# Optimization experiments

Hardware: AMD Instinct MI355X
Metric: run time of the kernel (lower is better)

Reference implementation:

```python
import jax, jax.numpy as jnp
import numpy as np
from jax import lax

K, INC, OUC = 6, 64, 32
H, W = 512, 512
WIN = 128  # min(128, min(H,W)) for training path
ITERATION = 2  # torch uses random.randint(1,3); fixed for determinism


def setup_inputs() -> dict:
    key = jax.random.key(0)
    ks = jax.random.split(key, 12)
    s = 0.05
    return {
        "x": jax.random.uniform(ks[0], (K, 3, H, W), jnp.float32),
        "pred_list": jax.random.uniform(ks[1], (K, 3, H, W), jnp.float32),
        "feat_list": jax.random.normal(ks[2], (K, INC, H, W), jnp.float32) * 0.1,
        "split_w": jax.random.normal(ks[3], (3 * OUC, INC, 3, 3), jnp.float32) * s,
        "split_b": jax.random.normal(ks[4], (3 * OUC,), jnp.float32) * s,
        "merge1_w": jax.random.normal(ks[5], (INC, 3 * OUC + 3, 3, 3), jnp.float32) * s,
        "merge1_b": jax.random.normal(ks[6], (INC,), jnp.float32) * s,
        "merge2_w": jax.random.normal(ks[7], (INC, INC, 3, 3), jnp.float32) * s,
        "merge2_b": jax.random.normal(ks[8], (INC,), jnp.float32) * s,
        "head_w": jax.random.normal(ks[9], (3, INC, 3, 3), jnp.float32) * s,
        "head_b": jax.random.normal(ks[10], (3,), jnp.float32) * s,
    }


def _conv(x, w, b, groups=1):
    y = lax.conv_general_dilated(
        x, w, (1, 1), ((1, 1), (1, 1)),
        dimension_numbers=("NCHW", "OIHW", "NCHW"), feature_group_count=groups)
    return y + b[None, :, None, None]


def _get_box(pred_list):
    # B_cat = mean of bg channel, T_cat = sum of fg channel; distance map [H,W]
    B_cat = pred_list[:, 2].mean(axis=0)
    T_cat = pred_list[:, 0].sum(axis=0)
    distance = jnp.abs(1.0 - T_cat - B_cat)
    # nearest-neighbor downsample by 0.1: out[i,j] = in[10*i, 10*j]
    hs, ws = H // 10, W // 10
    ds = distance[::10, ::10][:hs, :ws]
    # NMS keep[0] (training path uses boxes[0:1]) == global argmax of score
    idx = jnp.argmax(ds.reshape(-1))
    cx = (idx % ws) * 10
    cy = (idx // ws) * 10
    half = WIN // 2
    x1, y1 = cx - half, cy - half
    x2, y2 = cx + half, cy + half
    ox = (-jnp.minimum(x1, 0) + jnp.minimum(W - x1, 0)
          - jnp.minimum(x2, 0) + jnp.minimum(W - x2, 0))
    oy = (-jnp.minimum(y1, 0) + jnp.minimum(H - y1, 0)
          - jnp.minimum(y2, 0) + jnp.minimum(H - y2, 0))
    return (y1 + oy).astype(jnp.int32), (x1 + ox).astype(jnp.int32)


def reference(x, pred_list, feat_list, split_w, split_b,
              merge1_w, merge1_b, merge2_w, merge2_b, head_w, head_b):
    c = INC
    y1, x1 = _get_box(pred_list)  # box fixed across iterations (computed once)
    x_patch = lax.dynamic_slice(x, (0, 0, y1, x1), (K, 3, WIN, WIN))
    feat_patch = lax.dynamic_slice(feat_list, (0, 0, y1, x1), (K, INC, WIN, WIN))
    feat_tiled = jnp.tile(feat_patch, (1, 3, 1, 1))
    denom = max(K - 1, 1)

    pl = pred_list
    for _ in range(ITERATION):
        pred_patch = lax.dynamic_slice(pl, (0, 0, y1, x1), (K, 3, WIN, WIN))
        # cat([p0.repeat(c), p1.repeat(c), p2.repeat(c)]) == repeat each channel c times
        attention = jnp.repeat(pred_patch, c, axis=1)
        fs = _conv(feat_tiled * attention, split_w, split_b, groups=3)
        f0, f1, f2 = fs[:, :OUC], fs[:, OUC:2 * OUC], fs[:, 2 * OUC:]
        feat_t = f1.sum(0, keepdims=True) / denom - f0.sum(0, keepdims=True) + 2.0 * f0
        feat_r = f0.sum(0, keepdims=True) - f0 + f1
        feat_b = jnp.broadcast_to(f2.mean(0, keepdims=True), f2.shape)
        fcat = jnp.concatenate([feat_t, feat_r, feat_b, x_patch], axis=1)
        h1 = jax.nn.leaky_relu(_conv(fcat, merge1_w, merge1_b), 0.2)
        fm = _conv(h1, merge2_w, merge2_b)
        pr = _conv(fm, head_w, head_b)
        inner = (jnp.tanh(pr[:, :, 10:WIN - 10, 10:WIN - 10]) + 1.0) / 2.0
        pl = lax.dynamic_update_slice(pl, inner, (0, 0, y1 + 10, x1 + 10))
    return pl
```

## Files before the change

### kernel.cpp

```cpp
#include <hip/hip_runtime.h>
#include <math.h>

typedef __attribute__((ext_vector_type(8))) short short8_t;
typedef __attribute__((ext_vector_type(4))) float f32x4;

#define Hh 512
#define Ww 512
#define IMG (Hh * Ww)
#define WINP 128
#define PP (WINP * WINP)
#define QS 325

__device__ __forceinline__ unsigned short f2bf(float f) {
    unsigned int u = __builtin_bit_cast(unsigned int, f);
    u += 0x7fffu + ((u >> 16) & 1u);
    return (unsigned short)(u >> 16);
}
__device__ __forceinline__ float bf2f(unsigned short h) {
    unsigned int u = ((unsigned int)h) << 16;
    return __builtin_bit_cast(float, u);
}

__global__ void prologue_kernel(const float* __restrict__ pred, int* __restrict__ box,
                                const float* __restrict__ sw, const float* __restrict__ m1w,
                                const float* __restrict__ m2w, const float* __restrict__ hw,
                                unsigned short* __restrict__ WF,
                                const float4* __restrict__ csrc, float4* __restrict__ cdst)
{
    int b = blockIdx.x;
    int tid = threadIdx.x;
    if (b < 684) {
        int idx = b * 256 + tid;
        int j = idx & 7;
        int lane = (idx >> 3) & 63;
        int frag = idx >> 9;
        int n16 = lane & 15;
        int ko = (lane >> 4) * 8 + j;
        float v = 0.f;
        if (frag < 108) {
            int g = frag / 36; int r = frag % 36; int kc = r / 18; r %= 18; int tap = r / 2; int nf = r & 1;
            int oc = g * 32 + nf * 16 + n16; int ic = kc * 32 + ko;
            v = sw[(oc * 64 + ic) * 9 + tap];
        } else if (frag < 252) {
            int r = frag - 108; int half = r / 72; r %= 72; int kc = r / 18; r %= 18; int tap = r / 2; int nf = r & 1;
            int oc = half * 32 + nf * 16 + n16; int ic = kc * 32 + ko;
            if (ic < 99) v = m1w[(oc * 99 + ic) * 9 + tap];
        } else if (frag < 324) {
            int r = frag - 252; int half = r / 36; r %= 36; int kc = r / 18; r %= 18; int tap = r / 2; int nf = r & 1;
            int oc = half * 32 + nf * 16 + n16; int ic = kc * 32 + ko;
            v = m2w[(oc * 64 + ic) * 9 + tap];
        } else {
            int r = frag - 324; int kc = r / 9; int tap = r % 9;
            int ic = kc * 32 + ko;
            if (n16 < 3) v = hw[(n16 * 64 + ic) * 9 + tap];
        }
        WF[idx] = f2bf(v);
        return;
    }
    if (b < 5292) {
        int i = (b - 684) * 256 + tid;
        cdst[i] = csrc[i];
        return;
    }
    float best = -1.0f; int bidx = 0x7fffffff;
    for (int cand = tid; cand < 51 * 51; cand += 256) {
        int i = cand / 51, jj = cand % 51;
        int y = i * 10, x = jj * 10;
        float T = 0.f, Bv = 0.f;
#pragma unroll
        for (int k = 0; k < 6; ++k) {
            T  += pred[((k * 3 + 0) * Hh + y) * Ww + x];
            Bv += pred[((k * 3 + 2) * Hh + y) * Ww + x];
        }
        float d = fabsf(1.0f - T - Bv / 6.0f);
        if (d > best || (d == best && cand < bidx)) { best = d; bidx = cand; }
    }
    __shared__ float sv[256];
    __shared__ int   si[256];
    sv[tid] = best; si[tid] = bidx;
    __syncthreads();
    for (int s = 128; s > 0; s >>= 1) {
        if (tid < s) {
            if (sv[tid + s] > sv[tid] || (sv[tid + s] == sv[tid] && si[tid + s] < si[tid])) {
                sv[tid] = sv[tid + s]; si[tid] = si[tid + s];
            }
        }
        __syncthreads();
    }
    if (tid == 0) {
        int idx = si[0];
        int cy = (idx / 51) * 10, cx = (idx % 51) * 10;
        int yy = cy - 64; yy = yy < 0 ? 0 : (yy > Hh - WINP ? Hh - WINP : yy);
        int xx = cx - 64; xx = xx < 0 ? 0 : (xx > Ww - WINP ? Ww - WINP : xx);
        box[0] = yy; box[1] = xx;
    }
}

__global__ void prep_featcl(const float* __restrict__ feat, const int* __restrict__ box,
                            unsigned short* __restrict__ featcl)
{
    int row = blockIdx.x;
    int k = blockIdx.y;
    int t = threadIdx.x;
    int y1 = box[0], x1 = box[1];
    __shared__ unsigned short s[128 * 64];
    for (int i = 0; i < 32; ++i) {
        int idx = t + i * 256;
        int ic = idx >> 7, c = idx & 127;
        s[c * 64 + ic] = f2bf(feat[((size_t)(k * 64 + ic) * Hh + y1 + row) * Ww + x1 + c]);
    }
    __syncthreads();
    if (t < 128) {
        unsigned short* dst = &featcl[((size_t)k * 16384 + row * 128 + t) * 64];
        for (int i = 0; i < 8; ++i)
            *(short8_t*)&dst[i * 8] = *(short8_t*)&s[t * 64 + i * 8];
    }
}


__global__ __launch_bounds__(256) void split_mfma(
    const unsigned short* __restrict__ featcl, const float* __restrict__ pl,
    const unsigned short* __restrict__ WF, const float* __restrict__ sb,
    const int* __restrict__ box, unsigned short* __restrict__ fscl)
{
    const int tid = threadIdx.x;
    const int l = tid & 63, w = tid >> 6;
    const int T = blockIdx.x;
    const int k = blockIdx.y / 3, g = blockIdx.y % 3;
    const int ty0 = (T >> 3) * 16, tx0 = (T & 7) * 16;
    const int y1 = box[0], x1 = box[1];
    const int nf = w & 1;
    const int rbase = (w >> 1) * 8;

    __shared__ __align__(16) unsigned short s_a[4 * QS * 8];
    __shared__ __align__(16) unsigned short s_b[9216];

    f32x4 acc[8];
#pragma unroll
    for (int mf = 0; mf < 8; ++mf) acc[mf] = (f32x4){0.f, 0.f, 0.f, 0.f};

    const float* plg = pl + (size_t)(k * 3 + g) * IMG + (size_t)y1 * Ww + x1;
    const unsigned short* fck = featcl + (size_t)k * 16384 * 64;

    for (int kc = 0; kc < 2; ++kc) {
        __syncthreads();
#pragma unroll
        for (int i = 0; i < 6; ++i) {
            int s = tid + i * 256;
            if (s < 1296) {
                int pxs = s >> 2, q = s & 3;
                int r = pxs / 18, c = pxs - r * 18;
                int py = ty0 - 1 + r, px = tx0 - 1 + c;
                short8_t o;
                if (py >= 0 && py < WINP && px >= 0 && px < WINP) {
                    float pv = plg[py * Ww + px];
                    short8_t f = *(const short8_t*)&fck[(size_t)(py * WINP + px) * 64 + kc * 32 + q * 8];
#pragma unroll
                    for (int e = 0; e < 8; ++e) o[e] = (short)f2bf(bf2f((unsigned short)f[e]) * pv);
                } else {
#pragma unroll
                    for (int e = 0; e < 8; ++e) o[e] = 0;
                }
                *(short8_t*)&s_a[(q * QS + pxs) * 8] = o;
            }
        }
        {
            const unsigned short* src = WF + (size_t)((g * 2 + kc) * 18) * 512;
#pragma unroll
            for (int i = 0; i < 5; ++i) {
                int cch = tid + i * 256;
                if (cch < 1152)
                    *(short8_t*)&s_b[cch * 8] = *(const short8_t*)&src[cch * 8];
            }
        }
        __syncthreads();
        short8_t breg[9];
#pragma unroll
        for (int tap = 0; tap < 9; ++tap)
            breg[tap] = *(const short8_t*)&s_b[((tap * 2 + nf) * 64 + l) * 8];
#pragma unroll
        for (int r = 0; r < 10; ++r) {
            short8_t av[3];
#pragma unroll
            for (int dx = 0; dx < 3; ++dx)
                av[dx] = *(const short8_t*)&s_a[((l >> 4) * QS + (rbase + r) * 18 + (l & 15) + dx) * 8];
#pragma unroll
            for (int dy = 0; dy < 3; ++dy) {
                const int mf = r - dy;
                if (mf >= 0 && mf < 8) {
#pragma unroll
                    for (int dx = 0; dx < 3; ++dx)
                        acc[mf] = __builtin_amdgcn_mfma_f32_16x16x32_bf16(av[dx], breg[dy * 3 + dx], acc[mf], 0, 0, 0);
                }
            }
        }
    }
    __syncthreads();
    unsigned short* s_t = s_a;
    {
        float bias = sb[g * 32 + nf * 16 + (l & 15)];
        int slot = nf * 2 + ((l & 15) >> 3);
#pragma unroll
        for (int mf = 0; mf < 8; ++mf) {
            int row = rbase + mf;
#pragma unroll
            for (int r = 0; r < 4; ++r) {
                int col = (l >> 4) * 4 + r;
                s_t[(slot * 256 + row * 16 + col) * 8 + (l & 7)] = f2bf(acc[mf][r] + bias);
            }
        }
    }
    __syncthreads();
    {
        int row = tid >> 4, col = tid & 15;
        size_t gpx = (size_t)(ty0 + row) * WINP + tx0 + col;
        unsigned short* dst = fscl + ((size_t)k * 16384 + gpx) * 96 + g * 32;
#pragma unroll
        for (int i = 0; i < 4; ++i)
            *(short8_t*)&dst[i * 8] = *(short8_t*)&s_t[(i * 256 + tid) * 8];
    }
}

__global__ void reduce_kernel(const unsigned short* __restrict__ fscl, float* __restrict__ Scl)
{
    int tg = blockIdx.x * 256 + threadIdx.x;
    int px = tg >> 2, q = tg & 3;
    float s0[8], s1[8], s2[8];
#pragma unroll
    for (int e = 0; e < 8; ++e) { s0[e] = 0.f; s1[e] = 0.f; s2[e] = 0.f; }
#pragma unroll
    for (int k = 0; k < 6; ++k) {
        const unsigned short* p = &fscl[((size_t)k * 16384 + px) * 96 + q * 8];
        short8_t a0 = *(const short8_t*)&p[0];
        short8_t a1 = *(const short8_t*)&p[32];
        short8_t a2 = *(const short8_t*)&p[64];
#pragma unroll
        for (int e = 0; e < 8; ++e) {
            s0[e] += bf2f((unsigned short)a0[e]);
            s1[e] += bf2f((unsigned short)a1[e]);
            s2[e] += bf2f((unsigned short)a2[e]);
        }
    }
    float* d = &Scl[(size_t)px * 96 + q * 8];
#pragma unroll
    for (int e = 0; e < 8; ++e) {
        d[e]      = s1[e] * 0.2f - s0[e];
        d[32 + e] = s0[e];
        d[64 + e] = s2[e] * (1.f / 6.f);
    }
}

__global__ __launch_bounds__(256) void merge1_mfma(
    const unsigned short* __restrict__ fscl, const float* __restrict__ Scl,
    const float* __restrict__ x, const unsigned short* __restrict__ WF,
    const float* __restrict__ m1b, const int* __restrict__ box,
    unsigned short* __restrict__ h1cl)
{
    const int tid = threadIdx.x;
    const int l = tid & 63, w = tid >> 6;
    const int T = blockIdx.x;
    const int k = blockIdx.y >> 1, half = blockIdx.y & 1;
    const int ty0 = (T >> 3) * 16, tx0 = (T & 7) * 16;
    const int y1 = box[0], x1 = box[1];
    const int nf = w & 1;
    const int rbase = (w >> 1) * 8;

    __shared__ __align__(16) unsigned short s_a[4 * QS * 8];
    __shared__ __align__(16) unsigned short s_b[9216];

    f32x4 acc[8];
#pragma unroll
    for (int mf = 0; mf < 8; ++mf) acc[mf] = (f32x4){0.f, 0.f, 0.f, 0.f};

    for (int kc = 0; kc < 4; ++kc) {
        __syncthreads();
#pragma unroll
        for (int i = 0; i < 6; ++i) {
            int s = tid + i * 256;
            if (s < 1296) {
                int pxs = s >> 2, q = s & 3;
                int r = pxs / 18, c = pxs - r * 18;
                int py = ty0 - 1 + r, px = tx0 - 1 + c;
                short8_t o;
#pragma unroll
                for (int e = 0; e < 8; ++e) o[e] = 0;
                if (py >= 0 && py < WINP && px >= 0 && px < WINP) {
                    size_t gpx = (size_t)py * WINP + px;
                    if (kc == 0) {
                        short8_t f0 = *(const short8_t*)&fscl[((size_t)k * 16384 + gpx) * 96 + q * 8];
                        const float* S = &Scl[gpx * 96 + q * 8];
#pragma unroll
                        for (int e = 0; e < 8; ++e)
                            o[e] = (short)f2bf(S[e] + 2.f * bf2f((unsigned short)f0[e]));
                    } else if (kc == 1) {
                        const unsigned short* fp = &fscl[((size_t)k * 16384 + gpx) * 96];
                        short8_t f0 = *(const short8_t*)&fp[q * 8];
                        short8_t f1 = *(const short8_t*)&fp[32 + q * 8];
                        const float* S = &Scl[gpx * 96 + 32 + q * 8];
#pragma unroll
                        for (int e = 0; e < 8; ++e)
                            o[e] = (short)f2bf(S[e] - bf2f((unsigned short)f0[e]) + bf2f((unsigned short)f1[e]));
                    } else if (kc == 2) {
                        const float* S = &Scl[gpx * 96 + 64 + q * 8];
#pragma unroll
                        for (int e = 0; e < 8; ++e) o[e] = (short)f2bf(S[e]);
                    } else {
                        if (q == 0) {
#pragma unroll
                            for (int ch = 0; ch < 3; ++ch)
                                o[ch] = (short)f2bf(x[(size_t)(k * 3 + ch) * IMG + (size_t)(y1 + py) * Ww + x1 + px]);
                        }
                    }
                }
                *(short8_t*)&s_a[(q * QS + pxs) * 8] = o;
            }
        }
        {
            const unsigned short* src = WF + (size_t)(108 + (half * 4 + kc) * 18) * 512;
#pragma unroll
            for (int i = 0; i < 5; ++i) {
                int cch = tid + i * 256;
                if (cch < 1152)
                    *(short8_t*)&s_b[cch * 8] = *(const short8_t*)&src[cch * 8];
            }
        }
        __syncthreads();
        short8_t breg[9];
#pragma unroll
        for (int tap = 0; tap < 9; ++tap)
            breg[tap] = *(const short8_t*)&s_b[((tap * 2 + nf) * 64 + l) * 8];
#pragma unroll
        for (int r = 0; r < 10; ++r) {
            short8_t av[3];
#pragma unroll
            for (int dx = 0; dx < 3; ++dx)
                av[dx] = *(const short8_t*)&s_a[((l >> 4) * QS + (rbase + r) * 18 + (l & 15) + dx) * 8];
#pragma unroll
            for (int dy = 0; dy < 3; ++dy) {
                const int mf = r - dy;
                if (mf >= 0 && mf < 8) {
#pragma unroll
                    for (int dx = 0; dx < 3; ++dx)
                        acc[mf] = __builtin_amdgcn_mfma_f32_16x16x32_bf16(av[dx], breg[dy * 3 + dx], acc[mf], 0, 0, 0);
                }
            }
        }
    }
    __syncthreads();
    unsigned short* s_t = s_a;
    {
        float bias = m1b[half * 32 + nf * 16 + (l & 15)];
        int slot = nf * 2 + ((l & 15) >> 3);
#pragma unroll
        for (int mf = 0; mf < 8; ++mf) {
            int row = rbase + mf;
#pragma unroll
            for (int r = 0; r < 4; ++r) {
                int col = (l >> 4) * 4 + r;
                float v = acc[mf][r] + bias;
                v = v >= 0.f ? v : 0.2f * v;
                s_t[(slot * 256 + row * 16 + col) * 8 + (l & 7)] = f2bf(v);
            }
        }
    }
    __syncthreads();
    {
        int row = tid >> 4, col = tid & 15;
        size_t gpx = (size_t)(ty0 + row) * WINP + tx0 + col;
        unsigned short* dst = h1cl + ((size_t)k * 16384 + gpx) * 64 + half * 32;
#pragma unroll
        for (int i = 0; i < 4; ++i)
            *(short8_t*)&dst[i * 8] = *(short8_t*)&s_t[(i * 256 + tid) * 8];
    }
}

__global__ __launch_bounds__(256) void merge2_mfma(
    const unsigned short* __restrict__ h1cl, const unsigned short* __restrict__ WF,
    const float* __restrict__ m2b, unsigned short* __restrict__ h2cl)
{
    const int tid = threadIdx.x;
    const int l = tid & 63, w = tid >> 6;
    const int T = blockIdx.x;
    const int k = blockIdx.y >> 1, half = blockIdx.y & 1;
    const int ty0 = (T >> 3) * 16, tx0 = (T & 7) * 16;
    const int nf = w & 1;
    const int rbase = (w >> 1) * 8;

    __shared__ __align__(16) unsigned short s_a[4 * QS * 8];
    __shared__ __align__(16) unsigned short s_b[9216];

    f32x4 acc[8];
#pragma unroll
    for (int mf = 0; mf < 8; ++mf) acc[mf] = (f32x4){0.f, 0.f, 0.f, 0.f};

    const unsigned short* ink = h1cl + (size_t)k * 16384 * 64;

    for (int kc = 0; kc < 2; ++kc) {
        __syncthreads();
#pragma unroll
        for (int i = 0; i < 6; ++i) {
            int s = tid + i * 256;
            if (s < 1296) {
                int pxs = s >> 2, q = s & 3;
                int r = pxs / 18, c = pxs - r * 18;
                int py = ty0 - 1 + r, px = tx0 - 1 + c;
                short8_t o;
                if (py >= 0 && py < WINP && px >= 0 && px < WINP) {
                    o = *(const short8_t*)&ink[(size_t)(py * WINP + px) * 64 + kc * 32 + q * 8];
                } else {
#pragma unroll
                    for (int e = 0; e < 8; ++e) o[e] = 0;
                }
                *(short8_t*)&s_a[(q * QS + pxs) * 8] = o;
            }
        }
        {
            const unsigned short* src = WF + (size_t)(252 + (half * 2 + kc) * 18) * 512;
#pragma unroll
            for (int i = 0; i < 5; ++i) {
                int cch = tid + i * 256;
                if (cch < 1152)
                    *(short8_t*)&s_b[cch * 8] = *(const short8_t*)&src[cch * 8];
            }
        }
        __syncthreads();
        short8_t breg[9];
#pragma unroll
        for (int tap = 0; tap < 9; ++tap)
            breg[tap] = *(const short8_t*)&s_b[((tap * 2 + nf) * 64 + l) * 8];
#pragma unroll
        for (int r = 0; r < 10; ++r) {
            short8_t av[3];
#pragma unroll
            for (int dx = 0; dx < 3; ++dx)
                av[dx] = *(const short8_t*)&s_a[((l >> 4) * QS + (rbase + r) * 18 + (l & 15) + dx) * 8];
#pragma unroll
            for (int dy = 0; dy < 3; ++dy) {
                const int mf = r - dy;
                if (mf >= 0 && mf < 8) {
#pragma unroll
                    for (int dx = 0; dx < 3; ++dx)
                        acc[mf] = __builtin_amdgcn_mfma_f32_16x16x32_bf16(av[dx], breg[dy * 3 + dx], acc[mf], 0, 0, 0);
                }
            }
        }
    }
    __syncthreads();
    unsigned short* s_t = s_a;
    {
        float bias = m2b[half * 32 + nf * 16 + (l & 15)];
        int slot = nf * 2 + ((l & 15) >> 3);
#pragma unroll
        for (int mf = 0; mf < 8; ++mf) {
            int row = rbase + mf;
#pragma unroll
            for (int r = 0; r < 4; ++r) {
                int col = (l >> 4) * 4 + r;
                s_t[(slot * 256 + row * 16 + col) * 8 + (l & 7)] = f2bf(acc[mf][r] + bias);
            }
        }
    }
    __syncthreads();
    {
        int row = tid >> 4, col = tid & 15;
        size_t gpx = (size_t)(ty0 + row) * WINP + tx0 + col;
        unsigned short* dst = h2cl + ((size_t)k * 16384 + gpx) * 64 + half * 32;
#pragma unroll
        for (int i = 0; i < 4; ++i)
            *(short8_t*)&dst[i * 8] = *(short8_t*)&s_t[(i * 256 + tid) * 8];
    }
}

__global__ __launch_bounds__(256) void head_mfma(
    const unsigned short* __restrict__ h2cl, const unsigned short* __restrict__ WF,
    const float* __restrict__ hb, const int* __restrict__ box,
    float* __restrict__ out)
{
    const int tid = threadIdx.x;
    const int l = tid & 63, w = tid >> 6;
    const int T = blockIdx.x;
    const int k = blockIdx.y;
    const int oy0 = 10 + (T / 7) * 16, ox0 = 10 + (T % 7) * 16;
    const int y1 = box[0], x1 = box[1];

    __shared__ __align__(16) unsigned short s_a[4 * QS * 8];
    __shared__ __align__(16) unsigned short s_b[4608];

    f32x4 acc[4];
#pragma unroll
    for (int mf = 0; mf < 4; ++mf) acc[mf] = (f32x4){0.f, 0.f, 0.f, 0.f};

    const unsigned short* ink = h2cl + (size_t)k * 16384 * 64;

    for (int kc = 0; kc < 2; ++kc) {
        __syncthreads();
#pragma unroll
        for (int i = 0; i < 6; ++i) {
            int s = tid + i * 256;
            if (s < 1296) {
                int pxs = s >> 2, q = s & 3;
                int r = pxs / 18, c = pxs - r * 18;
                int py = oy0 - 1 + r, px = ox0 - 1 + c;
                *(short8_t*)&s_a[(q * QS + pxs) * 8] =
                    *(const short8_t*)&ink[(size_t)(py * WINP + px) * 64 + kc * 32 + q * 8];
            }
        }
        {
            const unsigned short* src = WF + (size_t)(324 + kc * 9) * 512;
#pragma unroll
            for (int i = 0; i < 3; ++i) {
                int cch = tid + i * 256;
                if (cch < 576)
                    *(short8_t*)&s_b[cch * 8] = *(const short8_t*)&src[cch * 8];
            }
        }
        __syncthreads();
        short8_t breg[9];
#pragma unroll
        for (int tap = 0; tap < 9; ++tap)
            breg[tap] = *(const short8_t*)&s_b[(tap * 64 + l) * 8];
#pragma unroll
        for (int r = 0; r < 6; ++r) {
            short8_t av[3];
#pragma unroll
            for (int dx = 0; dx < 3; ++dx)
                av[dx] = *(const short8_t*)&s_a[((l >> 4) * QS + (w * 4 + r) * 18 + (l & 15) + dx) * 8];
#pragma unroll
            for (int dy = 0; dy < 3; ++dy) {
                const int mf = r - dy;
                if (mf >= 0 && mf < 4) {
#pragma unroll
                    for (int dx = 0; dx < 3; ++dx)
                        acc[mf] = __builtin_amdgcn_mfma_f32_16x16x32_bf16(av[dx], breg[dy * 3 + dx], acc[mf], 0, 0, 0);
                }
            }
        }
    }
    int oc = l & 15;
    if (oc < 3) {
        float bias = hb[oc];
#pragma unroll
        for (int mf = 0; mf < 4; ++mf) {
            int row = oy0 + w * 4 + mf;
            if (row < 118) {
#pragma unroll
                for (int r = 0; r < 4; ++r) {
                    int col = ox0 + (l >> 4) * 4 + r;
                    if (col < 118) {
                        float v = (tanhf(acc[mf][r] + bias) + 1.0f) * 0.5f;
                        out[(size_t)(k * 3 + oc) * IMG + (size_t)(y1 + row) * Ww + x1 + col] = v;
                    }
                }
            }
        }
    }
}

extern "C" void kernel_launch(void* const* d_in, const int* in_sizes, int n_in,
                              void* d_out, int out_size, void* d_ws, size_t ws_size,
                              hipStream_t stream)
{
    const float* x       = (const float*)d_in[0];
    const float* pred    = (const float*)d_in[1];
    const float* feat    = (const float*)d_in[2];
    const float* split_w = (const float*)d_in[3];
    const float* split_b = (const float*)d_in[4];
    const float* m1w     = (const float*)d_in[5];
    const float* m1b     = (const float*)d_in[6];
    const float* m2w     = (const float*)d_in[7];
    const float* m2b     = (const float*)d_in[8];
    const float* hw      = (const float*)d_in[9];
    const float* hb      = (const float*)d_in[10];
    float* out = (float*)d_out;

    char* base = (char*)d_ws;
    size_t o = 0;
    int* box = (int*)(base + o);                  o += 256;
    unsigned short* WF = (unsigned short*)(base + o);      o += (size_t)175104 * 2;  o = (o + 255) & ~(size_t)255;
    unsigned short* featcl = (unsigned short*)(base + o);  o += (size_t)6 * 16384 * 64 * 2;
    unsigned short* fscl = (unsigned short*)(base + o);    o += (size_t)6 * 16384 * 96 * 2;
    float* Scl = (float*)(base + o);                       o += (size_t)16384 * 96 * 4;
    unsigned short* h1cl = (unsigned short*)(base + o);    o += (size_t)6 * 16384 * 64 * 2;
    unsigned short* h2cl = (unsigned short*)(base + o);    o += (size_t)6 * 16384 * 64 * 2;

    prologue_kernel<<<5293, 256, 0, stream>>>(pred, box, split_w, m1w, m2w, hw, WF,
                                              (const float4*)pred, (float4*)out);
    prep_featcl<<<dim3(128, 6), 256, 0, stream>>>(feat, box, featcl);

    for (int it = 0; it < 2; ++it) {
        split_mfma<<<dim3(64, 18), 256, 0, stream>>>(featcl, out, WF, split_b, box, fscl);
        reduce_kernel<<<256, 256, 0, stream>>>(fscl, Scl);
        merge1_mfma<<<dim3(64, 12), 256, 0, stream>>>(fscl, Scl, x, WF, m1b, box, h1cl);
        merge2_mfma<<<dim3(64, 12), 256, 0, stream>>>(h1cl, WF, m2b, h2cl);
        head_mfma<<<dim3(49, 6), 256, 0, stream>>>(h2cl, WF, hb, box, out);
    }
}
```

Measured before the change: 658.3 us.

## Fuse all stages into one persistent kernel with software grid barriers

Replaces the sequence of twelve kernel launches (prologue, feature prep, and five per-iteration conv/reduce stages) with a single persistent kernel of 768 blocks. Stages are separated by an atomic-counter grid barrier, and the box is recomputed redundantly in every block instead of being stored to global memory. This removes launch overheads and inter-kernel gaps. In exchange it relies on all 768 blocks being co-resident (launch bounds of 3 blocks per CU), which risks deadlock otherwise, and it adds spin-barrier costs plus redundant argmax work in every block.

```diff
diff --git a/kernel.cpp b/kernel.cpp
--- a/kernel.cpp
+++ b/kernel.cpp
@@ -8,8 +8,8 @@
 #define Ww 512
 #define IMG (Hh * Ww)
 #define WINP 128
-#define PP (WINP * WINP)
 #define QS 325
+#define NBLK 768
 
 __device__ __forceinline__ unsigned short f2bf(float f) {
     unsigned int u = __builtin_bit_cast(unsigned int, f);
@@ -21,538 +21,556 @@
     return __builtin_bit_cast(float, u);
 }
 
-__global__ void prologue_kernel(const float* __restrict__ pred, int* __restrict__ box,
-                                const float* __restrict__ sw, const float* __restrict__ m1w,
-                                const float* __restrict__ m2w, const float* __restrict__ hw,
-                                unsigned short* __restrict__ WF,
-                                const float4* __restrict__ csrc, float4* __restrict__ cdst)
+__device__ __forceinline__ void gbar(unsigned int* bar) {
+    __syncthreads();
+    if (threadIdx.x == 0) {
+        __threadfence();
+        unsigned g = atomicAdd(&bar[1], 0u);
+        unsigned arrived = atomicAdd(&bar[0], 1u);
+        if (arrived == NBLK - 1u) {
+            atomicSub(&bar[0], (unsigned)NBLK);
+            atomicAdd(&bar[1], 1u);
+        } else {
+            while (atomicAdd(&bar[1], 0u) == g)
+                __builtin_amdgcn_s_sleep(1);
+        }
+        __threadfence();
+    }
+    __syncthreads();
+}
+
+__global__ __launch_bounds__(256, 3) void mega_kernel(
+    const float* __restrict__ x, const float* __restrict__ pred,
+    const float* __restrict__ feat,
+    const float* __restrict__ sw, const float* __restrict__ sbias,
+    const float* __restrict__ m1w, const float* __restrict__ m1b,
+    const float* __restrict__ m2w, const float* __restrict__ m2b,
+    const float* __restrict__ hw, const float* __restrict__ hb,
+    float* __restrict__ out,
+    unsigned int* __restrict__ bar,
+    unsigned short* __restrict__ WF, unsigned short* __restrict__ featcl,
+    unsigned short* __restrict__ fscl, float* __restrict__ Scl,
+    unsigned short* __restrict__ h1cl, unsigned short* __restrict__ h2cl)
 {
-    int b = blockIdx.x;
-    int tid = threadIdx.x;
-    if (b < 684) {
-        int idx = b * 256 + tid;
-        int j = idx & 7;
-        int lane = (idx >> 3) & 63;
-        int frag = idx >> 9;
-        int n16 = lane & 15;
-        int ko = (lane >> 4) * 8 + j;
-        float v = 0.f;
-        if (frag < 108) {
-            int g = frag / 36; int r = frag % 36; int kc = r / 18; r %= 18; int tap = r / 2; int nf = r & 1;
-            int oc = g * 32 + nf * 16 + n16; int ic = kc * 32 + ko;
-            v = sw[(oc * 64 + ic) * 9 + tap];
-        } else if (frag < 252) {
-            int r = frag - 108; int half = r / 72; r %= 72; int kc = r / 18; r %= 18; int tap = r / 2; int nf = r & 1;
-            int oc = half * 32 + nf * 16 + n16; int ic = kc * 32 + ko;
-            if (ic < 99) v = m1w[(oc * 99 + ic) * 9 + tap];
-        } else if (frag < 324) {
-            int r = frag - 252; int half = r / 36; r %= 36; int kc = r / 18; r %= 18; int tap = r / 2; int nf = r & 1;
-            int oc = half * 32 + nf * 16 + n16; int ic = kc * 32 + ko;
-            v = m2w[(oc * 64 + ic) * 9 + tap];
-        } else {
-            int r = frag - 324; int kc = r / 9; int tap = r % 9;
-            int ic = kc * 32 + ko;
-            if (n16 < 3) v = hw[(n16 * 64 + ic) * 9 + tap];
-        }
-        WF[idx] = f2bf(v);
-        return;
-    }
-    if (b < 5292) {
-        int i = (b - 684) * 256 + tid;
-        cdst[i] = csrc[i];
-        return;
-    }
-    float best = -1.0f; int bidx = 0x7fffffff;
-    for (int cand = tid; cand < 51 * 51; cand += 256) {
-        int i = cand / 51, jj = cand % 51;
-        int y = i * 10, x = jj * 10;
-        float T = 0.f, Bv = 0.f;
-#pragma unroll
-        for (int k = 0; k < 6; ++k) {
-            T  += pred[((k * 3 + 0) * Hh + y) * Ww + x];
-            Bv += pred[((k * 3 + 2) * Hh + y) * Ww + x];
-        }
-        float d = fabsf(1.0f - T - Bv / 6.0f);
-        if (d > best || (d == best && cand < bidx)) { best = d; bidx = cand; }
-    }
-    __shared__ float sv[256];
-    __shared__ int   si[256];
-    sv[tid] = best; si[tid] = bidx;
-    __syncthreads();
-    for (int s = 128; s > 0; s >>= 1) {
-        if (tid < s) {
-            if (sv[tid + s] > sv[tid] || (sv[tid + s] == sv[tid] && si[tid + s] < si[tid])) {
-                sv[tid] = sv[tid + s]; si[tid] = si[tid + s];
-            }
-        }
+    const int tid = threadIdx.x;
+    const int bx = blockIdx.x;
+    const int l = tid & 63, w = tid >> 6;
+    const int nf = w & 1;
+    const int rbase = (w >> 1) * 8;
+
+    __shared__ __align__(16) unsigned short s_a[4 * QS * 8];
+    __shared__ __align__(16) unsigned short s_b[9216];
+
+    int y1, x1;
+    {
+        float best = -1.0f; int bidx = 0x7fffffff;
+        for (int cand = tid; cand < 51 * 51; cand += 256) {
+            int i = cand / 51, jj = cand % 51;
+            int y = i * 10, xx = jj * 10;
+            float T = 0.f, Bv = 0.f;
+#pragma unroll
+            for (int k = 0; k < 6; ++k) {
+                T  += pred[((k * 3 + 0) * Hh + y) * Ww + xx];
+                Bv += pred[((k * 3 + 2) * Hh + y) * Ww + xx];
+            }
+            float d = fabsf(1.0f - T - Bv / 6.0f);
+            if (d > best || (d == best && cand < bidx)) { best = d; bidx = cand; }
+        }
+        float* sv = (float*)s_b;
+        int*   si = (int*)(s_b + 512);
+        int*   sres = (int*)(s_b + 1024);
+        sv[tid] = best; si[tid] = bidx;
+        __syncthreads();
+        for (int s = 128; s > 0; s >>= 1) {
+            if (tid < s) {
+                if (sv[tid + s] > sv[tid] || (sv[tid + s] == sv[tid] && si[tid + s] < si[tid])) {
+                    sv[tid] = sv[tid + s]; si[tid] = si[tid + s];
+                }
+            }
+            __syncthreads();
+        }
+        if (tid == 0) {
+            int idx = si[0];
+            int cy = (idx / 51) * 10, cx = (idx % 51) * 10;
+            int yy = cy - 64; yy = yy < 0 ? 0 : (yy > Hh - WINP ? Hh - WINP : yy);
+            int xx = cx - 64; xx = xx < 0 ? 0 : (xx > Ww - WINP ? Ww - WINP : xx);
+            sres[0] = yy; sres[1] = xx;
+        }
+        __syncthreads();
+        y1 = sres[0]; x1 = sres[1];
         __syncthreads();
     }
-    if (tid == 0) {
-        int idx = si[0];
-        int cy = (idx / 51) * 10, cx = (idx % 51) * 10;
-        int yy = cy - 64; yy = yy < 0 ? 0 : (yy > Hh - WINP ? Hh - WINP : yy);
-        int xx = cx - 64; xx = xx < 0 ? 0 : (xx > Ww - WINP ? Ww - WINP : xx);
-        box[0] = yy; box[1] = xx;
+
+    for (int u = bx; u < 6060; u += NBLK) {
+        if (u < 684) {
+            int idx = u * 256 + tid;
+            int j = idx & 7;
+            int lane = (idx >> 3) & 63;
+            int frag = idx >> 9;
+            int n16 = lane & 15;
+            int ko = (lane >> 4) * 8 + j;
+            float v = 0.f;
+            if (frag < 108) {
+                int g = frag / 36; int r = frag % 36; int kc = r / 18; r %= 18; int tap = r / 2; int nff = r & 1;
+                int oc = g * 32 + nff * 16 + n16; int ic = kc * 32 + ko;
+                v = sw[(oc * 64 + ic) * 9 + tap];
+            } else if (frag < 252) {
+                int r = frag - 108; int half = r / 72; r %= 72; int kc = r / 18; r %= 18; int tap = r / 2; int nff = r & 1;
+                int oc = half * 32 + nff * 16 + n16; int ic = kc * 32 + ko;
+                if (ic < 99) v = m1w[(oc * 99 + ic) * 9 + tap];
+            } else if (frag < 324) {
+                int r = frag - 252; int half = r / 36; r %= 36; int kc = r / 18; r %= 18; int tap = r / 2; int nff = r & 1;
+                int oc = half * 32 + nff * 16 + n16; int ic = kc * 32 + ko;
+                v = m2w[(oc * 64 + ic) * 9 + tap];
+            } else {
+                int r = frag - 324; int kc = r / 9; int tap = r % 9;
+                int ic = kc * 32 + ko;
+                if (n16 < 3) v = hw[(n16 * 64 + ic) * 9 + tap];
+            }
+            WF[idx] = f2bf(v);
+        } else if (u < 5292) {
+            int i = (u - 684) * 256 + tid;
+            ((float4*)out)[i] = ((const float4*)pred)[i];
+        } else {
+            int fu = u - 5292;
+            int row = fu & 127, k = fu >> 7;
+            __syncthreads();
+            for (int i = 0; i < 32; ++i) {
+                int idx = tid + i * 256;
+                int ic = idx >> 7, c = idx & 127;
+                s_a[c * 64 + ic] = f2bf(feat[((size_t)(k * 64 + ic) * Hh + y1 + row) * Ww + x1 + c]);
+            }
+            __syncthreads();
+            if (tid < 128) {
+                unsigned short* dst = &featcl[((size_t)k * 16384 + row * 128 + tid) * 64];
+                for (int i = 0; i < 8; ++i)
+                    *(short8_t*)&dst[i * 8] = *(short8_t*)&s_a[tid * 64 + i * 8];
+            }
+        }
     }
-}
-
-__global__ void prep_featcl(const float* __restrict__ feat, const int* __restrict__ box,
-                            unsigned short* __restrict__ featcl)
-{
-    int row = blockIdx.x;
-    int k = blockIdx.y;
-    int t = threadIdx.x;
-    int y1 = box[0], x1 = box[1];
-    __shared__ unsigned short s[128 * 64];
-    for (int i = 0; i < 32; ++i) {
-        int idx = t + i * 256;
-        int ic = idx >> 7, c = idx & 127;
-        s[c * 64 + ic] = f2bf(feat[((size_t)(k * 64 + ic) * Hh + y1 + row) * Ww + x1 + c]);
-    }
-    __syncthreads();
-    if (t < 128) {
-        unsigned short* dst = &featcl[((size_t)k * 16384 + row * 128 + t) * 64];
-        for (int i = 0; i < 8; ++i)
-            *(short8_t*)&dst[i * 8] = *(short8_t*)&s[t * 64 + i * 8];
-    }
-}
-
-
-__global__ __launch_bounds__(256) void split_mfma(
-    const unsigned short* __restrict__ featcl, const float* __restrict__ pl,
-    const unsigned short* __restrict__ WF, const float* __restrict__ sb,
-    const int* __restrict__ box, unsigned short* __restrict__ fscl)
-{
-    const int tid = threadIdx.x;
-    const int l = tid & 63, w = tid >> 6;
-    const int T = blockIdx.x;
-    const int k = blockIdx.y / 3, g = blockIdx.y % 3;
-    const int ty0 = (T >> 3) * 16, tx0 = (T & 7) * 16;
-    const int y1 = box[0], x1 = box[1];
-    const int nf = w & 1;
-    const int rbase = (w >> 1) * 8;
-
-    __shared__ __align__(16) unsigned short s_a[4 * QS * 8];
-    __shared__ __align__(16) unsigned short s_b[9216];
-
-    f32x4 acc[8];
-#pragma unroll
-    for (int mf = 0; mf < 8; ++mf) acc[mf] = (f32x4){0.f, 0.f, 0.f, 0.f};
-
-    const float* plg = pl + (size_t)(k * 3 + g) * IMG + (size_t)y1 * Ww + x1;
-    const unsigned short* fck = featcl + (size_t)k * 16384 * 64;
-
-    for (int kc = 0; kc < 2; ++kc) {
-        __syncthreads();
-#pragma unroll
-        for (int i = 0; i < 6; ++i) {
-            int s = tid + i * 256;
-            if (s < 1296) {
-                int pxs = s >> 2, q = s & 3;
-                int r = pxs / 18, c = pxs - r * 18;
-                int py = ty0 - 1 + r, px = tx0 - 1 + c;
-                short8_t o;
-                if (py >= 0 && py < WINP && px >= 0 && px < WINP) {
-                    float pv = plg[py * Ww + px];
-                    short8_t f = *(const short8_t*)&fck[(size_t)(py * WINP + px) * 64 + kc * 32 + q * 8];
-#pragma unroll
-                    for (int e = 0; e < 8; ++e) o[e] = (short)f2bf(bf2f((unsigned short)f[e]) * pv);
-                } else {
-#pragma unroll
-                    for (int e = 0; e < 8; ++e) o[e] = 0;
-                }
-                *(short8_t*)&s_a[(q * QS + pxs) * 8] = o;
-            }
-        }
+    gbar(bar);
+
+    for (int it = 0; it < 2; ++it) {
+        for (int u = bx; u < 1152; u += NBLK) {
+            const int T = u & 63;
+            const int ky = u >> 6;
+            const int k = ky / 3, g = ky % 3;
+            const int ty0 = (T >> 3) * 16, tx0 = (T & 7) * 16;
+
+            f32x4 acc[8];
+#pragma unroll
+            for (int mf = 0; mf < 8; ++mf) acc[mf] = (f32x4){0.f, 0.f, 0.f, 0.f};
+
+            const float* plg = out + (size_t)(k * 3 + g) * IMG + (size_t)y1 * Ww + x1;
+            const unsigned short* fck = featcl + (size_t)k * 16384 * 64;
+
+            for (int kc = 0; kc < 2; ++kc) {
+                __syncthreads();
+#pragma unroll
+                for (int i = 0; i < 6; ++i) {
+                    int s = tid + i * 256;
+                    if (s < 1296) {
+                        int pxs = s >> 2, q = s & 3;
+                        int r = pxs / 18, c = pxs - r * 18;
+                        int py = ty0 - 1 + r, px = tx0 - 1 + c;
+                        short8_t o;
+                        if (py >= 0 && py < WINP && px >= 0 && px < WINP) {
+                            float pv = plg[py * Ww + px];
+                            short8_t f = *(const short8_t*)&fck[(size_t)(py * WINP + px) * 64 + kc * 32 + q * 8];
+#pragma unroll
+                            for (int e = 0; e < 8; ++e) o[e] = (short)f2bf(bf2f((unsigned short)f[e]) * pv);
+                        } else {
+#pragma unroll
+                            for (int e = 0; e < 8; ++e) o[e] = 0;
+                        }
+                        *(short8_t*)&s_a[(q * QS + pxs) * 8] = o;
+                    }
+                }
+                {
+                    const unsigned short* src = WF + (size_t)((g * 2 + kc) * 18) * 512;
+#pragma unroll
+                    for (int i = 0; i < 5; ++i) {
+                        int cch = tid + i * 256;
+                        if (cch < 1152)
+                            *(short8_t*)&s_b[cch * 8] = *(const short8_t*)&src[cch * 8];
+                    }
+                }
+                __syncthreads();
+                short8_t breg[9];
+#pragma unroll
+                for (int tap = 0; tap < 9; ++tap)
+                    breg[tap] = *(const short8_t*)&s_b[((tap * 2 + nf) * 64 + l) * 8];
+#pragma unroll
+                for (int r = 0; r < 10; ++r) {
+                    short8_t av[3];
+#pragma unroll
+                    for (int dx = 0; dx < 3; ++dx)
+                        av[dx] = *(const short8_t*)&s_a[((l >> 4) * QS + (rbase + r) * 18 + (l & 15) + dx) * 8];
+#pragma unroll
+                    for (int dy = 0; dy < 3; ++dy) {
+                        const int mf = r - dy;
+                        if (mf >= 0 && mf < 8) {
+#pragma unroll
+                            for (int dx = 0; dx < 3; ++dx)
+                                acc[mf] = __builtin_amdgcn_mfma_f32_16x16x32_bf16(av[dx], breg[dy * 3 + dx], acc[mf], 0, 0, 0);
+                        }
+                    }
+                }
+            }
+            __syncthreads();
+            {
+                float bias = sbias[g * 32 + nf * 16 + (l & 15)];
+                int slot = nf * 2 + ((l & 15) >> 3);
+#pragma unroll
+                for (int mf = 0; mf < 8; ++mf) {
+                    int row = rbase + mf;
+#pragma unroll
+                    for (int r = 0; r < 4; ++r) {
+                        int col = (l >> 4) * 4 + r;
+                        s_a[(slot * 256 + row * 16 + col) * 8 + (l & 7)] = f2bf(acc[mf][r] + bias);
+                    }
+                }
+            }
+            __syncthreads();
+            {
+                int row = tid >> 4, col = tid & 15;
+                size_t gpx = (size_t)(ty0 + row) * WINP + tx0 + col;
+                unsigned short* dst = fscl + ((size_t)k * 16384 + gpx) * 96 + g * 32;
+#pragma unroll
+                for (int i = 0; i < 4; ++i)
+                    *(short8_t*)&dst[i * 8] = *(short8_t*)&s_a[(i * 256 + tid) * 8];
+            }
+        }
+        gbar(bar);
+
         {
-            const unsigned short* src = WF + (size_t)((g * 2 + kc) * 18) * 512;
-#pragma unroll
-            for (int i = 0; i < 5; ++i) {
-                int cch = tid + i * 256;
-                if (cch < 1152)
-                    *(short8_t*)&s_b[cch * 8] = *(const short8_t*)&src[cch * 8];
-            }
-        }
-        __syncthreads();
-        short8_t breg[9];
-#pragma unroll
-        for (int tap = 0; tap < 9; ++tap)
-            breg[tap] = *(const short8_t*)&s_b[((tap * 2 + nf) * 64 + l) * 8];
-#pragma unroll
-        for (int r = 0; r < 10; ++r) {
-            short8_t av[3];
-#pragma unroll
-            for (int dx = 0; dx < 3; ++dx)
-                av[dx] = *(const short8_t*)&s_a[((l >> 4) * QS + (rbase + r) * 18 + (l & 15) + dx) * 8];
-#pragma unroll
-            for (int dy = 0; dy < 3; ++dy) {
-                const int mf = r - dy;
-                if (mf >= 0 && mf < 8) {
+            int gidx = bx * 256 + tid;
+            int p = gidx >> 16;
+            int tg = gidx & 65535;
+            int px = tg >> 2, q = tg & 3;
+            float* d = &Scl[(size_t)px * 96 + q * 8];
+            if (p == 0) {
+                float s0[8], s1[8];
+#pragma unroll
+                for (int e = 0; e < 8; ++e) { s0[e] = 0.f; s1[e] = 0.f; }
+#pragma unroll
+                for (int k = 0; k < 6; ++k) {
+                    const unsigned short* pp = &fscl[((size_t)k * 16384 + px) * 96 + q * 8];
+                    short8_t a0 = *(const short8_t*)&pp[0];
+                    short8_t a1 = *(const short8_t*)&pp[32];
+#pragma unroll
+                    for (int e = 0; e < 8; ++e) {
+                        s0[e] += bf2f((unsigned short)a0[e]);
+                        s1[e] += bf2f((unsigned short)a1[e]);
+                    }
+                }
+#pragma unroll
+                for (int e = 0; e < 8; ++e) d[e] = s1[e] * 0.2f - s0[e];
+            } else if (p == 1) {
+                float s0[8];
+#pragma unroll
+                for (int e = 0; e < 8; ++e) s0[e] = 0.f;
+#pragma unroll
+                for (int k = 0; k < 6; ++k) {
+                    const unsigned short* pp = &fscl[((size_t)k * 16384 + px) * 96 + q * 8];
+                    short8_t a0 = *(const short8_t*)&pp[0];
+#pragma unroll
+                    for (int e = 0; e < 8; ++e) s0[e] += bf2f((unsigned short)a0[e]);
+                }
+#pragma unroll
+                for (int e = 0; e < 8; ++e) d[32 + e] = s0[e];
+            } else {
+                float s2[8];
+#pragma unroll
+                for (int e = 0; e < 8; ++e) s2[e] = 0.f;
+#pragma unroll
+                for (int k = 0; k < 6; ++k) {
+                    const unsigned short* pp = &fscl[((size_t)k * 16384 + px) * 96 + q * 8];
+                    short8_t a2 = *(const short8_t*)&pp[64];
+#pragma unroll
+                    for (int e = 0; e < 8; ++e) s2[e] += bf2f((unsigned short)a2[e]);
+                }
+#pragma unroll
+                for (int e = 0; e < 8; ++e) d[64 + e] = s2[e] * (1.f / 6.f);
+            }
+        }
+        gbar(bar);
+
+        {
+            const int T = bx & 63;
+            const int ky = bx >> 6;
+            const int k = ky >> 1, half = ky & 1;
+            const int ty0 = (T >> 3) * 16, tx0 = (T & 7) * 16;
+
+            f32x4 acc[8];
+#pragma unroll
+            for (int mf = 0; mf < 8; ++mf) acc[mf] = (f32x4){0.f, 0.f, 0.f, 0.f};
+
+            for (int kc = 0; kc < 4; ++kc) {
+                __syncthreads();
+#pragma unroll
+                for (int i = 0; i < 6; ++i) {
+                    int s = tid + i * 256;
+                    if (s < 1296) {
+                        int pxs = s >> 2, q = s & 3;
+                        int r = pxs / 18, c = pxs - r * 18;
+                        int py = ty0 - 1 + r, px = tx0 - 1 + c;
+                        short8_t o;
+#pragma unroll
+                        for (int e = 0; e < 8; ++e) o[e] = 0;
+                        if (py >= 0 && py < WINP && px >= 0 && px < WINP) {
+                            size_t gpx = (size_t)py * WINP + px;
+                            if (kc == 0) {
+                                short8_t f0 = *(const short8_t*)&fscl[((size_t)k * 16384 + gpx) * 96 + q * 8];
+                                const float* S = &Scl[gpx * 96 + q * 8];
+#pragma unroll
+                                for (int e = 0; e < 8; ++e)
+                                    o[e] = (short)f2bf(S[e] + 2.f * bf2f((unsigned short)f0[e]));
+                            } else if (kc == 1) {
+                                const unsigned short* fp = &fscl[((size_t)k * 16384 + gpx) * 96];
+                                short8_t f0 = *(const short8_t*)&fp[q * 8];
+                                short8_t f1 = *(const short8_t*)&fp[32 + q * 8];
+                                const float* S = &Scl[gpx * 96 + 32 + q * 8];
+#pragma unroll
+                                for (int e = 0; e < 8; ++e)
+                                    o[e] = (short)f2bf(S[e] - bf2f((unsigned short)f0[e]) + bf2f((unsigned short)f1[e]));
+                            } else if (kc == 2) {
+                                const float* S = &Scl[gpx * 96 + 64 + q * 8];
+#pragma unroll
+                                for (int e = 0; e < 8; ++e) o[e] = (short)f2bf(S[e]);
+                            } else {
+                                if (q == 0) {
+#pragma unroll
+                                    for (int ch = 0; ch < 3; ++ch)
+                                        o[ch] = (short)f2bf(x[(size_t)(k * 3 + ch) * IMG + (size_t)(y1 + py) * Ww + x1 + px]);
+                                }
+                            }
+                        }
+                        *(short8_t*)&s_a[(q * QS + pxs) * 8] = o;
+                    }
+                }
+                {
+                    const unsigned short* src = WF + (size_t)(108 + (half * 4 + kc) * 18) * 512;
+#pragma unroll
+                    for (int i = 0; i < 5; ++i) {
+                        int cch = tid + i * 256;
+                        if (cch < 1152)
+                            *(short8_t*)&s_b[cch * 8] = *(const short8_t*)&src[cch * 8];
+                    }
+                }
+                __syncthreads();
+                short8_t breg[9];
+#pragma unroll
+                for (int tap = 0; tap < 9; ++tap)
+                    breg[tap] = *(const short8_t*)&s_b[((tap * 2 + nf) * 64 + l) * 8];
+#pragma unroll
+                for (int r = 0; r < 10; ++r) {
+                    short8_t av[3];
 #pragma unroll
                     for (int dx = 0; dx < 3; ++dx)
-                        acc[mf] = __builtin_amdgcn_mfma_f32_16x16x32_bf16(av[dx], breg[dy * 3 + dx], acc[mf], 0, 0, 0);
-                }
-            }
-        }
-    }
-    __syncthreads();
-    unsigned short* s_t = s_a;
-    {
-        float bias = sb[g * 32 + nf * 16 + (l & 15)];
-        int slot = nf * 2 + ((l & 15) >> 3);
-#pragma unroll
-        for (int mf = 0; mf < 8; ++mf) {
-            int row = rbase + mf;
-#pragma unroll
-            for (int r = 0; r < 4; ++r) {
-                int col = (l >> 4) * 4 + r;
-                s_t[(slot * 256 + row * 16 + col) * 8 + (l & 7)] = f2bf(acc[mf][r] + bias);
-            }
-        }
-    }
-    __syncthreads();
-    {
-        int row = tid >> 4, col = tid & 15;
-        size_t gpx = (size_t)(ty0 + row) * WINP + tx0 + col;
-        unsigned short* dst = fscl + ((size_t)k * 16384 + gpx) * 96 + g * 32;
-#pragma unroll
-        for (int i = 0; i < 4; ++i)
-            *(short8_t*)&dst[i * 8] = *(short8_t*)&s_t[(i * 256 + tid) * 8];
-    }
-}
-
-__global__ void reduce_kernel(const unsigned short* __restrict__ fscl, float* __restrict__ Scl)
-{
-    int tg = blockIdx.x * 256 + threadIdx.x;
-    int px = tg >> 2, q = tg & 3;
-    float s0[8], s1[8], s2[8];
-#pragma unroll
-    for (int e = 0; e < 8; ++e) { s0[e] = 0.f; s1[e] = 0.f; s2[e] = 0.f; }
-#pragma unroll
-    for (int k = 0; k < 6; ++k) {
-        const unsigned short* p = &fscl[((size_t)k * 16384 + px) * 96 + q * 8];
-        short8_t a0 = *(const short8_t*)&p[0];
-        short8_t a1 = *(const short8_t*)&p[32];
-        short8_t a2 = *(const short8_t*)&p[64];
-#pragma unroll
-        for (int e = 0; e < 8; ++e) {
-            s0[e] += bf2f((unsigned short)a0[e]);
-            s1[e] += bf2f((unsigned short)a1[e]);
-            s2[e] += bf2f((unsigned short)a2[e]);
-        }
-    }
-    float* d = &Scl[(size_t)px * 96 + q * 8];
-#pragma unroll
-    for (int e = 0; e < 8; ++e) {
-        d[e]      = s1[e] * 0.2f - s0[e];
-        d[32 + e] = s0[e];
-        d[64 + e] = s2[e] * (1.f / 6.f);
-    }
-}
-
-__global__ __launch_bounds__(256) void merge1_mfma(
-    const unsigned short* __restrict__ fscl, const float* __restrict__ Scl,
-    const float* __restrict__ x, const unsigned short* __restrict__ WF,
-    const float* __restrict__ m1b, const int* __restrict__ box,
-    unsigned short* __restrict__ h1cl)
-{
-    const int tid = threadIdx.x;
-    const int l = tid & 63, w = tid >> 6;
-    const int T = blockIdx.x;
-    const int k = blockIdx.y >> 1, half = blockIdx.y & 1;
-    const int ty0 = (T >> 3) * 16, tx0 = (T & 7) * 16;
-    const int y1 = box[0], x1 = box[1];
-    const int nf = w & 1;
-    const int rbase = (w >> 1) * 8;
-
-    __shared__ __align__(16) unsigned short s_a[4 * QS * 8];
-    __shared__ __align__(16) unsigned short s_b[9216];
-
-    f32x4 acc[8];
-#pragma unroll
-    for (int mf = 0; mf < 8; ++mf) acc[mf] = (f32x4){0.f, 0.f, 0.f, 0.f};
-
-    for (int kc = 0; kc < 4; ++kc) {
-        __syncthreads();
-#pragma unroll
-        for (int i = 0; i < 6; ++i) {
-            int s = tid + i * 256;
-            if (s < 1296) {
-                int pxs = s >> 2, q = s & 3;
-                int r = pxs / 18, c = pxs - r * 18;
-                int py = ty0 - 1 + r, px = tx0 - 1 + c;
-                short8_t o;
-#pragma unroll
-                for (int e = 0; e < 8; ++e) o[e] = 0;
-                if (py >= 0 && py < WINP && px >= 0 && px < WINP) {
-                    size_t gpx = (size_t)py * WINP + px;
-                    if (kc == 0) {
-                        short8_t f0 = *(const short8_t*)&fscl[((size_t)k * 16384 + gpx) * 96 + q * 8];
-                        const float* S = &Scl[gpx * 96 + q * 8];
-#pragma unroll
-                        for (int e = 0; e < 8; ++e)
-                            o[e] = (short)f2bf(S[e] + 2.f * bf2f((unsigned short)f0[e]));
-                    } else if (kc == 1) {
-                        const unsigned short* fp = &fscl[((size_t)k * 16384 + gpx) * 96];
-                        short8_t f0 = *(const short8_t*)&fp[q * 8];
-                        short8_t f1 = *(const short8_t*)&fp[32 + q * 8];
-                        const float* S = &Scl[gpx * 96 + 32 + q * 8];
-#pragma unroll
-                        for (int e = 0; e < 8; ++e)
-                            o[e] = (short)f2bf(S[e] - bf2f((unsigned short)f0[e]) + bf2f((unsigned short)f1[e]));
-                    } else if (kc == 2) {
-                        const float* S = &Scl[gpx * 96 + 64 + q * 8];
-#pragma unroll
-                        for (int e = 0; e < 8; ++e) o[e] = (short)f2bf(S[e]);
-                    } else {
-                        if (q == 0) {
-#pragma unroll
-                            for (int ch = 0; ch < 3; ++ch)
-                                o[ch] = (short)f2bf(x[(size_t)(k * 3 + ch) * IMG + (size_t)(y1 + py) * Ww + x1 + px]);
-                        }
-                    }
-                }
-                *(short8_t*)&s_a[(q * QS + pxs) * 8] = o;
-            }
-        }
+                        av[dx] = *(const short8_t*)&s_a[((l >> 4) * QS + (rbase + r) * 18 + (l & 15) + dx) * 8];
+#pragma unroll
+                    for (int dy = 0; dy < 3; ++dy) {
+                        const int mf = r - dy;
+                        if (mf >= 0 && mf < 8) {
+#pragma unroll
+                            for (int dx = 0; dx < 3; ++dx)
+                                acc[mf] = __builtin_amdgcn_mfma_f32_16x16x32_bf16(av[dx], breg[dy * 3 + dx], acc[mf], 0, 0, 0);
+                        }
+                    }
+                }
+            }
+            __syncthreads();
+            {
+                float bias = m1b[half * 32 + nf * 16 + (l & 15)];
+                int slot = nf * 2 + ((l & 15) >> 3);
+#pragma unroll
+                for (int mf = 0; mf < 8; ++mf) {
+                    int row = rbase + mf;
+#pragma unroll
+                    for (int r = 0; r < 4; ++r) {
+                        int col = (l >> 4) * 4 + r;
+                        float v = acc[mf][r] + bias;
+                        v = v >= 0.f ? v : 0.2f * v;
+                        s_a[(slot * 256 + row * 16 + col) * 8 + (l & 7)] = f2bf(v);
+                    }
+                }
+            }
+            __syncthreads();
+            {
+                int row = tid >> 4, col = tid & 15;
+                size_t gpx = (size_t)(ty0 + row) * WINP + tx0 + col;
+                unsigned short* dst = h1cl + ((size_t)k * 16384 + gpx) * 64 + half * 32;
+#pragma unroll
+                for (int i = 0; i < 4; ++i)
+                    *(short8_t*)&dst[i * 8] = *(short8_t*)&s_a[(i * 256 + tid) * 8];
+            }
+        }
+        gbar(bar);
+
         {
-            const unsigned short* src = WF + (size_t)(108 + (half * 4 + kc) * 18) * 512;
-#pragma unroll
-            for (int i = 0; i < 5; ++i) {
-                int cch = tid + i * 256;
-                if (cch < 1152)
-                    *(short8_t*)&s_b[cch * 8] = *(const short8_t*)&src[cch * 8];
-            }
-        }
-        __syncthreads();
-        short8_t breg[9];
-#pragma unroll
-        for (int tap = 0; tap < 9; ++tap)
-            breg[tap] = *(const short8_t*)&s_b[((tap * 2 + nf) * 64 + l) * 8];
-#pragma unroll
-        for (int r = 0; r < 10; ++r) {
-            short8_t av[3];
-#pragma unroll
-            for (int dx = 0; dx < 3; ++dx)
-                av[dx] = *(const short8_t*)&s_a[((l >> 4) * QS + (rbase + r) * 18 + (l & 15) + dx) * 8];
-#pragma unroll
-            for (int dy = 0; dy < 3; ++dy) {
-                const int mf = r - dy;
-                if (mf >= 0 && mf < 8) {
+            const int T = bx & 63;
+            const int ky = bx >> 6;
+            const int k = ky >> 1, half = ky & 1;
+            const int ty0 = (T >> 3) * 16, tx0 = (T & 7) * 16;
+
+            f32x4 acc[8];
+#pragma unroll
+            for (int mf = 0; mf < 8; ++mf) acc[mf] = (f32x4){0.f, 0.f, 0.f, 0.f};
+
+            const unsigned short* ink = h1cl + (size_t)k * 16384 * 64;
+
+            for (int kc = 0; kc < 2; ++kc) {
+                __syncthreads();
+#pragma unroll
+                for (int i = 0; i < 6; ++i) {
+                    int s = tid + i * 256;
+                    if (s < 1296) {
+                        int pxs = s >> 2, q = s & 3;
+                        int r = pxs / 18, c = pxs - r * 18;
+                        int py = ty0 - 1 + r, px = tx0 - 1 + c;
+                        short8_t o;
+                        if (py >= 0 && py < WINP && px >= 0 && px < WINP) {
+                            o = *(const short8_t*)&ink[(size_t)(py * WINP + px) * 64 + kc * 32 + q * 8];
+                        } else {
+#pragma unroll
+                            for (int e = 0; e < 8; ++e) o[e] = 0;
+                        }
+                        *(short8_t*)&s_a[(q * QS + pxs) * 8] = o;
+                    }
+                }
+                {
+                    const unsigned short* src = WF + (size_t)(252 + (half * 2 + kc) * 18) * 512;
+#pragma unroll
+                    for (int i = 0; i < 5; ++i) {
+                        int cch = tid + i * 256;
+                        if (cch < 1152)
+                            *(short8_t*)&s_b[cch * 8] = *(const short8_t*)&src[cch * 8];
+                    }
+                }
+                __syncthreads();
+                short8_t breg[9];
+#pragma unroll
+                for (int tap = 0; tap < 9; ++tap)
+                    breg[tap] = *(const short8_t*)&s_b[((tap * 2 + nf) * 64 + l) * 8];
+#pragma unroll
+                for (int r = 0; r < 10; ++r) {
+                    short8_t av[3];
 #pragma unroll
                     for (int dx = 0; dx < 3; ++dx)
-                        acc[mf] = __builtin_amdgcn_mfma_f32_16x16x32_bf16(av[dx], breg[dy * 3 + dx], acc[mf], 0, 0, 0);
-                }
-            }
-        }
-    }
-    __syncthreads();
-    unsigned short* s_t = s_a;
-    {
-        float bias = m1b[half * 32 + nf * 16 + (l & 15)];
-        int slot = nf * 2 + ((l & 15) >> 3);
-#pragma unroll
-        for (int mf = 0; mf < 8; ++mf) {
-            int row = rbase + mf;
-#pragma unroll
-            for (int r = 0; r < 4; ++r) {
-                int col = (l >> 4) * 4 + r;
-                float v = acc[mf][r] + bias;
-                v = v >= 0.f ? v : 0.2f * v;
-                s_t[(slot * 256 + row * 16 + col) * 8 + (l & 7)] = f2bf(v);
-            }
-        }
-    }
-    __syncthreads();
-    {
-        int row = tid >> 4, col = tid & 15;
-        size_t gpx = (size_t)(ty0 + row) * WINP + tx0 + col;
-        unsigned short* dst = h1cl + ((size_t)k * 16384 + gpx) * 64 + half * 32;
-#pragma unroll
-        for (int i = 0; i < 4; ++i)
-            *(short8_t*)&dst[i * 8] = *(short8_t*)&s_t[(i * 256 + tid) * 8];
-    }
-}
-
-__global__ __launch_bounds__(256) void merge2_mfma(
-    const unsigned short* __restrict__ h1cl, const unsigned short* __restrict__ WF,
-    const float* __restrict__ m2b, unsigned short* __restrict__ h2cl)
-{
-    const int tid = threadIdx.x;
-    const int l = tid & 63, w = tid >> 6;
-    const int T = blockIdx.x;
-    const int k = blockIdx.y >> 1, half = blockIdx.y & 1;
-    const int ty0 = (T >> 3) * 16, tx0 = (T & 7) * 16;
-    const int nf = w & 1;
-    const int rbase = (w >> 1) * 8;
-
-    __shared__ __align__(16) unsigned short s_a[4 * QS * 8];
-    __shared__ __align__(16) unsigned short s_b[9216];
-
-    f32x4 acc[8];
-#pragma unroll
-    for (int mf = 0; mf < 8; ++mf) acc[mf] = (f32x4){0.f, 0.f, 0.f, 0.f};
-
-    const unsigned short* ink = h1cl + (size_t)k * 16384 * 64;
-
-    for (int kc = 0; kc < 2; ++kc) {
-        __syncthreads();
-#pragma unroll
-        for (int i = 0; i < 6; ++i) {
-            int s = tid + i * 256;
-            if (s < 1296) {
-                int pxs = s >> 2, q = s & 3;
-                int r = pxs / 18, c = pxs - r * 18;
-                int py = ty0 - 1 + r, px = tx0 - 1 + c;
-                short8_t o;
-                if (py >= 0 && py < WINP && px >= 0 && px < WINP) {
-                    o = *(const short8_t*)&ink[(size_t)(py * WINP + px) * 64 + kc * 32 + q * 8];
-                } else {
-#pragma unroll
-                    for (int e = 0; e < 8; ++e) o[e] = 0;
-                }
-                *(short8_t*)&s_a[(q * QS + pxs) * 8] = o;
-            }
-        }
-        {
-            const unsigned short* src = WF + (size_t)(252 + (half * 2 + kc) * 18) * 512;
-#pragma unroll
-            for (int i = 0; i < 5; ++i) {
-                int cch = tid + i * 256;
-                if (cch < 1152)
-                    *(short8_t*)&s_b[cch * 8] = *(const short8_t*)&src[cch * 8];
-            }
-        }
-        __syncthreads();
-        short8_t breg[9];
-#pragma unroll
-        for (int tap = 0; tap < 9; ++tap)
-            breg[tap] = *(const short8_t*)&s_b[((tap * 2 + nf) * 64 + l) * 8];
-#pragma unroll
-        for (int r = 0; r < 10; ++r) {
-            short8_t av[3];
-#pragma unroll
-            for (int dx = 0; dx < 3; ++dx)
-                av[dx] = *(const short8_t*)&s_a[((l >> 4) * QS + (rbase + r) * 18 + (l & 15) + dx) * 8];
-#pragma unroll
-            for (int dy = 0; dy < 3; ++dy) {
-                const int mf = r - dy;
-                if (mf >= 0 && mf < 8) {
+                        av[dx] = *(const short8_t*)&s_a[((l >> 4) * QS + (rbase + r) * 18 + (l & 15) + dx) * 8];
+#pragma unroll
+                    for (int dy = 0; dy < 3; ++dy) {
+                        const int mf = r - dy;
+                        if (mf >= 0 && mf < 8) {
+#pragma unroll
+                            for (int dx = 0; dx < 3; ++dx)
+                                acc[mf] = __builtin_amdgcn_mfma_f32_16x16x32_bf16(av[dx], breg[dy * 3 + dx], acc[mf], 0, 0, 0);
+                        }
+                    }
+                }
+            }
+            __syncthreads();
+            {
+                float bias = m2b[half * 32 + nf * 16 + (l & 15)];
+                int slot = nf * 2 + ((l & 15) >> 3);
+#pragma unroll
+                for (int mf = 0; mf < 8; ++mf) {
+                    int row = rbase + mf;
+#pragma unroll
+                    for (int r = 0; r < 4; ++r) {
+                        int col = (l >> 4) * 4 + r;
+                        s_a[(slot * 256 + row * 16 + col) * 8 + (l & 7)] = f2bf(acc[mf][r] + bias);
+                    }
+                }
+            }
+            __syncthreads();
+            {
+                int row = tid >> 4, col = tid & 15;
+                size_t gpx = (size_t)(ty0 + row) * WINP + tx0 + col;
+                unsigned short* dst = h2cl + ((size_t)k * 16384 + gpx) * 64 + half * 32;
+#pragma unroll
+                for (int i = 0; i < 4; ++i)
+                    *(short8_t*)&dst[i * 8] = *(short8_t*)&s_a[(i * 256 + tid) * 8];
+            }
+        }
+        gbar(bar);
+
+        if (bx < 294) {
+            const int T = bx % 49;
+            const int k = bx / 49;
+            const int oy0 = 10 + (T / 7) * 16, ox0 = 10 + (T % 7) * 16;
+
+            f32x4 acc[4];
+#pragma unroll
+            for (int mf = 0; mf < 4; ++mf) acc[mf] = (f32x4){0.f, 0.f, 0.f, 0.f};
+
+            const unsigned short* ink = h2cl + (size_t)k * 16384 * 64;
+
+            for (int kc = 0; kc < 2; ++kc) {
+                __syncthreads();
+#pragma unroll
+                for (int i = 0; i < 6; ++i) {
+                    int s = tid + i * 256;
+                    if (s < 1296) {
+                        int pxs = s >> 2, q = s & 3;
+                        int r = pxs / 18, c = pxs - r * 18;
+                        int py = oy0 - 1 + r, px = ox0 - 1 + c;
+                        *(short8_t*)&s_a[(q * QS + pxs) * 8] =
+                            *(const short8_t*)&ink[(size_t)(py * WINP + px) * 64 + kc * 32 + q * 8];
+                    }
+                }
+                {
+                    const unsigned short* src = WF + (size_t)(324 + kc * 9) * 512;
+#pragma unroll
+                    for (int i = 0; i < 3; ++i) {
+                        int cch = tid + i * 256;
+                        if (cch < 576)
+                            *(short8_t*)&s_b[cch * 8] = *(const short8_t*)&src[cch * 8];
+                    }
+                }
+                __syncthreads();
+                short8_t breg[9];
+#pragma unroll
+                for (int tap = 0; tap < 9; ++tap)
+                    breg[tap] = *(const short8_t*)&s_b[(tap * 64 + l) * 8];
+#pragma unroll
+                for (int r = 0; r < 6; ++r) {
+                    short8_t av[3];
 #pragma unroll
                     for (int dx = 0; dx < 3; ++dx)
-                        acc[mf] = __builtin_amdgcn_mfma_f32_16x16x32_bf16(av[dx], breg[dy * 3 + dx], acc[mf], 0, 0, 0);
-                }
-            }
-        }
-    }
-    __syncthreads();
-    unsigned short* s_t = s_a;
-    {
-        float bias = m2b[half * 32 + nf * 16 + (l & 15)];
-        int slot = nf * 2 + ((l & 15) >> 3);
-#pragma unroll
-        for (int mf = 0; mf < 8; ++mf) {
-            int row = rbase + mf;
-#pragma unroll
-            for (int r = 0; r < 4; ++r) {
-                int col = (l >> 4) * 4 + r;
-                s_t[(slot * 256 + row * 16 + col) * 8 + (l & 7)] = f2bf(acc[mf][r] + bias);
-            }
-        }
-    }
-    __syncthreads();
-    {
-        int row = tid >> 4, col = tid & 15;
-        size_t gpx = (size_t)(ty0 + row) * WINP + tx0 + col;
-        unsigned short* dst = h2cl + ((size_t)k * 16384 + gpx) * 64 + half * 32;
-#pragma unroll
-        for (int i = 0; i < 4; ++i)
-            *(short8_t*)&dst[i * 8] = *(short8_t*)&s_t[(i * 256 + tid) * 8];
-    }
-}
-
-__global__ __launch_bounds__(256) void head_mfma(
-    const unsigned short* __restrict__ h2cl, const unsigned short* __restrict__ WF,
-    const float* __restrict__ hb, const int* __restrict__ box,
-    float* __restrict__ out)
-{
-    const int tid = threadIdx.x;
-    const int l = tid & 63, w = tid >> 6;
-    const int T = blockIdx.x;
-    const int k = blockIdx.y;
-    const int oy0 = 10 + (T / 7) * 16, ox0 = 10 + (T % 7) * 16;
-    const int y1 = box[0], x1 = box[1];
-
-    __shared__ __align__(16) unsigned short s_a[4 * QS * 8];
-    __shared__ __align__(16) unsigned short s_b[4608];
-
-    f32x4 acc[4];
-#pragma unroll
-    for (int mf = 0; mf < 4; ++mf) acc[mf] = (f32x4){0.f, 0.f, 0.f, 0.f};
-
-    const unsigned short* ink = h2cl + (size_t)k * 16384 * 64;
-
-    for (int kc = 0; kc < 2; ++kc) {
-        __syncthreads();
-#pragma unroll
-        for (int i = 0; i < 6; ++i) {
-            int s = tid + i * 256;
-            if (s < 1296) {
-                int pxs = s >> 2, q = s & 3;
-                int r = pxs / 18, c = pxs - r * 18;
-                int py = oy0 - 1 + r, px = ox0 - 1 + c;
-                *(short8_t*)&s_a[(q * QS + pxs) * 8] =
-                    *(const short8_t*)&ink[(size_t)(py * WINP + px) * 64 + kc * 32 + q * 8];
-            }
-        }
-        {
-            const unsigned short* src = WF + (size_t)(324 + kc * 9) * 512;
-#pragma unroll
-            for (int i = 0; i < 3; ++i) {
-                int cch = tid + i * 256;
-                if (cch < 576)
-                    *(short8_t*)&s_b[cch * 8] = *(const short8_t*)&src[cch * 8];
-            }
-        }
-        __syncthreads();
-        short8_t breg[9];
-#pragma unroll
-        for (int tap = 0; tap < 9; ++tap)
-            breg[tap] = *(const short8_t*)&s_b[(tap * 64 + l) * 8];
-#pragma unroll
-        for (int r = 0; r < 6; ++r) {
-            short8_t av[3];
-#pragma unroll
-            for (int dx = 0; dx < 3; ++dx)
-                av[dx] = *(const short8_t*)&s_a[((l >> 4) * QS + (w * 4 + r) * 18 + (l & 15) + dx) * 8];
-#pragma unroll
-            for (int dy = 0; dy < 3; ++dy) {
-                const int mf = r - dy;
-                if (mf >= 0 && mf < 4) {
-#pragma unroll
-                    for (int dx = 0; dx < 3; ++dx)
-                        acc[mf] = __builtin_amdgcn_mfma_f32_16x16x32_bf16(av[dx], breg[dy * 3 + dx], acc[mf], 0, 0, 0);
-                }
-            }
-        }
-    }
-    int oc = l & 15;
-    if (oc < 3) {
-        float bias = hb[oc];
-#pragma unroll
-        for (int mf = 0; mf < 4; ++mf) {
-            int row = oy0 + w * 4 + mf;
-            if (row < 118) {
-#pragma unroll
-                for (int r = 0; r < 4; ++r) {
-                    int col = ox0 + (l >> 4) * 4 + r;
-                    if (col < 118) {
-                        float v = (tanhf(acc[mf][r] + bias) + 1.0f) * 0.5f;
-                        out[(size_t)(k * 3 + oc) * IMG + (size_t)(y1 + row) * Ww + x1 + col] = v;
-                    }
-                }
-            }
-        }
+                        av[dx] = *(const short8_t*)&s_a[((l >> 4) * QS + (w * 4 + r) * 18 + (l & 15) + dx) * 8];
+#pragma unroll
+                    for (int dy = 0; dy < 3; ++dy) {
+                        const int mf = r - dy;
+                        if (mf >= 0 && mf < 4) {
+#pragma unroll
+                            for (int dx = 0; dx < 3; ++dx)
+                                acc[mf] = __builtin_amdgcn_mfma_f32_16x16x32_bf16(av[dx], breg[dy * 3 + dx], acc[mf], 0, 0, 0);
+                        }
+                    }
+                }
+            }
+            int oc = l & 15;
+            if (oc < 3) {
+                float bias = hb[oc];
+#pragma unroll
+                for (int mf = 0; mf < 4; ++mf) {
+                    int row = oy0 + w * 4 + mf;
+                    if (row < 118) {
+#pragma unroll
+                        for (int r = 0; r < 4; ++r) {
+                            int col = ox0 + (l >> 4) * 4 + r;
+                            if (col < 118) {
+                                float v = (tanhf(acc[mf][r] + bias) + 1.0f) * 0.5f;
+                                out[(size_t)(k * 3 + oc) * IMG + (size_t)(y1 + row) * Ww + x1 + col] = v;
+                            }
+                        }
+                    }
+                }
+            }
+        }
+        if (it == 0) gbar(bar);
     }
 }
 
@@ -575,7 +593,7 @@
 
     char* base = (char*)d_ws;
     size_t o = 0;
-    int* box = (int*)(base + o);                  o += 256;
+    unsigned int* bar = (unsigned int*)(base + o);         o += 256;
     unsigned short* WF = (unsigned short*)(base + o);      o += (size_t)175104 * 2;  o = (o + 255) & ~(size_t)255;
     unsigned short* featcl = (unsigned short*)(base + o);  o += (size_t)6 * 16384 * 64 * 2;
     unsigned short* fscl = (unsigned short*)(base + o);    o += (size_t)6 * 16384 * 96 * 2;
@@ -583,15 +601,9 @@
     unsigned short* h1cl = (unsigned short*)(base + o);    o += (size_t)6 * 16384 * 64 * 2;
     unsigned short* h2cl = (unsigned short*)(base + o);    o += (size_t)6 * 16384 * 64 * 2;
 
-    prologue_kernel<<<5293, 256, 0, stream>>>(pred, box, split_w, m1w, m2w, hw, WF,
-                                              (const float4*)pred, (float4*)out);
-    prep_featcl<<<dim3(128, 6), 256, 0, stream>>>(feat, box, featcl);
-
-    for (int it = 0; it < 2; ++it) {
-        split_mfma<<<dim3(64, 18), 256, 0, stream>>>(featcl, out, WF, split_b, box, fscl);
-        reduce_kernel<<<256, 256, 0, stream>>>(fscl, Scl);
-        merge1_mfma<<<dim3(64, 12), 256, 0, stream>>>(fscl, Scl, x, WF, m1b, box, h1cl);
-        merge2_mfma<<<dim3(64, 12), 256, 0, stream>>>(h1cl, WF, m2b, h2cl);
-        head_mfma<<<dim3(49, 6), 256, 0, stream>>>(h2cl, WF, hb, box, out);
-    }
+    hipMemsetAsync(bar, 0, 256, stream);
+
+    mega_kernel<<<dim3(NBLK), dim3(256), 0, stream>>>(
+        x, pred, feat, split_w, split_b, m1w, m1b, m2w, m2b, hw, hb,
+        out, bar, WF, featcl, fscl, Scl, h1cl, h2cl);
 }
```

Measured after the change: 1.855 ms. 2.82x slower.
